# Performance work log

Measured on AMD Instinct MI355X. Metric: run time of the kernel, lower is better.

Reference implementation:

```python
import jax, jax.numpy as jnp
import numpy as np

B, LC, LQ, D = 64, 512, 64, 256

def setup_inputs() -> dict:
    key = jax.random.key(0)
    k1, k2, k3, k4 = jax.random.split(key, 4)
    contex = jax.random.normal(k1, (B, LC, D), dtype=jnp.float32)
    question = jax.random.normal(k2, (B, LQ, D), dtype=jnp.float32)
    W_weight = jax.random.normal(k3, (1, 3 * D), dtype=jnp.float32) * (1.0 / np.sqrt(3 * D))
    W_bias = jax.random.normal(k4, (1,), dtype=jnp.float32) * 0.01
    return {"contex": contex, "question": question, "W_weight": W_weight, "W_bias": W_bias}

def reference(contex, question, W_weight, W_bias):
    d = contex.shape[-1]
    w = W_weight[0]  # [3D]; cat order in original is [q, c, q*c]
    wq, wc, wi = w[:d], w[d:2 * d], w[2 * d:]
    # S[b,i,j] = c_i.wc + q_j.wq + (c_i*q_j).wi + bias  (trilinear decomposition)
    s_c = contex @ wc                                   # [B, Lc]
    s_q = question @ wq                                 # [B, Lq]
    s_i = jnp.einsum('bid,bjd->bij', contex * wi, question)  # [B, Lc, Lq]
    S = s_i + s_c[:, :, None] + s_q[:, None, :] + W_bias[0]
    S1 = jax.nn.softmax(S, axis=2)                      # over question
    S2 = jax.nn.softmax(S, axis=1)                      # over context
    A = jnp.einsum('bij,bjd->bid', S1, question)        # [B, Lc, D]
    S3 = jnp.einsum('bij,bkj->bik', S1, S2)             # [B, Lc, Lc]
    Bm = jnp.einsum('bik,bkd->bid', S3, contex)         # [B, Lc, D]
    out = jnp.concatenate([contex, A, contex * A, contex * Bm], axis=2)  # [B, Lc, 4D]
    return out  # dropout is identity at inference
```

## Files before the change

kernel.cpp:

```cpp
#include <hip/hip_runtime.h>

#define BB 64
#define LCC 512
#define LQQ 64
#define DDD 256

typedef short bf16x8 __attribute__((ext_vector_type(8)));
typedef float f32x4 __attribute__((ext_vector_type(4)));

static __device__ __forceinline__ unsigned short f2bf(float f) {
  union { float f; unsigned u; } v; v.f = f;
  unsigned u = v.u;
  return (unsigned short)((u + 0x7fffu + ((u >> 16) & 1u)) >> 16);
}
static __device__ __forceinline__ float bf2f(unsigned u16) {
  union { unsigned u; float f; } v; v.u = (u16 & 0xffffu) << 16;
  return v.f;
}

__global__ __launch_bounds__(256) void k1_scores(
    const float* __restrict__ cx, const float* __restrict__ qu,
    const float* __restrict__ W, const float* __restrict__ Wb,
    unsigned short* __restrict__ E, unsigned short* __restrict__ Et,
    float* __restrict__ rinv)
{
  __shared__ float w_lds[768];
  __shared__ unsigned short Bs[64 * 264];
  __shared__ float E_lds[64 * 65];
  __shared__ float red[256];
  __shared__ float sc_lds[64];
  __shared__ float sq_lds[64];

  const int tid = threadIdx.x;
  const int b  = blockIdx.x >> 3;
  const int i0 = (blockIdx.x & 7) * 64;
  const int w = tid >> 6, lane = tid & 63, quad = lane >> 4, ln = lane & 15;

  for (int idx = tid; idx < 768; idx += 256) w_lds[idx] = W[idx];
  __syncthreads();

  {
    const int bj = tid >> 2, bc = tid & 3;
    const float4* src = (const float4*)(qu + ((size_t)(b * LQQ + bj)) * DDD + bc * 64);
    const float* wq = w_lds + bc * 64;
    unsigned short* dst = Bs + bj * 264 + bc * 64;
    float sqp = 0.f;
#pragma unroll
    for (int u = 0; u < 16; ++u) {
      float4 v = src[u];
      sqp += v.x * wq[u*4+0] + v.y * wq[u*4+1] + v.z * wq[u*4+2] + v.w * wq[u*4+3];
      ushort4 o = { f2bf(v.x), f2bf(v.y), f2bf(v.z), f2bf(v.w) };
      *(ushort4*)(dst + u * 4) = o;
    }
    red[tid] = sqp;
  }
  __syncthreads();
  if (tid < 64) sq_lds[tid] = red[4*tid] + red[4*tid+1] + red[4*tid+2] + red[4*tid+3];

  f32x4 acc[4];
#pragma unroll
  for (int c = 0; c < 4; ++c) acc[c] = (f32x4){0.f, 0.f, 0.f, 0.f};

  float scp = 0.f;
  const float* cxrow = cx + ((size_t)(b * LCC + i0 + w * 16 + ln)) * DDD;
#pragma unroll
  for (int kk = 0; kk < 4; ++kk)
#pragma unroll
    for (int ks = 0; ks < 2; ++ks) {
      const int k0 = kk * 64 + ks * 32 + quad * 8;
      float4 c0 = *(const float4*)(cxrow + k0);
      float4 c1 = *(const float4*)(cxrow + k0 + 4);
      const float* wcp = w_lds + 256 + k0;
      const float* wip = w_lds + 512 + k0;
      scp += c0.x*wcp[0] + c0.y*wcp[1] + c0.z*wcp[2] + c0.w*wcp[3]
           + c1.x*wcp[4] + c1.y*wcp[5] + c1.z*wcp[6] + c1.w*wcp[7];
      bf16x8 af;
      af[0] = (short)f2bf(c0.x * wip[0]);
      af[1] = (short)f2bf(c0.y * wip[1]);
      af[2] = (short)f2bf(c0.z * wip[2]);
      af[3] = (short)f2bf(c0.w * wip[3]);
      af[4] = (short)f2bf(c1.x * wip[4]);
      af[5] = (short)f2bf(c1.y * wip[5]);
      af[6] = (short)f2bf(c1.z * wip[6]);
      af[7] = (short)f2bf(c1.w * wip[7]);
#pragma unroll
      for (int tn = 0; tn < 4; ++tn) {
        bf16x8 bf = *(const bf16x8*)(Bs + (tn * 16 + ln) * 264 + k0);
        acc[tn] = __builtin_amdgcn_mfma_f32_16x16x32_bf16(af, bf, acc[tn], 0, 0, 0);
      }
    }

  __syncthreads();
  red[(w * 16 + ln) * 4 + quad] = scp;
  __syncthreads();
  if (tid < 64)
    sc_lds[tid] = red[4*tid] + red[4*tid+1] + red[4*tid+2] + red[4*tid+3] + Wb[0];
  __syncthreads();

#pragma unroll
  for (int tn = 0; tn < 4; ++tn)
#pragma unroll
    for (int r = 0; r < 4; ++r) {
      int il = w * 16 + quad * 4 + r;
      int j  = tn * 16 + ln;
      E_lds[il * 65 + j] = __expf(acc[tn][r] + sc_lds[il] + sq_lds[j]);
    }
  __syncthreads();
  {
    const int i = tid >> 2, c = tid & 3;
    float s = 0.f;
#pragma unroll
    for (int j = 0; j < 16; ++j) s += E_lds[i * 65 + c * 16 + j];
    red[tid] = s;
  }
  __syncthreads();
  if (tid < 64)
    rinv[b * LCC + i0 + tid] = 1.0f / (red[4*tid] + red[4*tid+1] + red[4*tid+2] + red[4*tid+3]);

  {
    const int i = tid >> 2, c = tid & 3;
    unsigned short* dst = E + ((size_t)(b * LCC + i0 + i)) * 64 + c * 16;
    const float* srcr = E_lds + i * 65 + c * 16;
#pragma unroll
    for (int u = 0; u < 4; ++u) {
      ushort4 o = { f2bf(srcr[u*4+0]), f2bf(srcr[u*4+1]), f2bf(srcr[u*4+2]), f2bf(srcr[u*4+3]) };
      *(ushort4*)(dst + u * 4) = o;
    }
  }
  {
    const int j = tid >> 2, c = tid & 3;
    unsigned short* dst = Et + ((size_t)(b * LQQ + j)) * LCC + i0 + c * 16;
#pragma unroll
    for (int u = 0; u < 4; ++u) {
      ushort4 o;
      o.x = f2bf(E_lds[(c*16 + u*4 + 0) * 65 + j]);
      o.y = f2bf(E_lds[(c*16 + u*4 + 1) * 65 + j]);
      o.z = f2bf(E_lds[(c*16 + u*4 + 2) * 65 + j]);
      o.w = f2bf(E_lds[(c*16 + u*4 + 3) * 65 + j]);
      *(ushort4*)(dst + u * 4) = o;
    }
  }
}

__global__ __launch_bounds__(256) void k2_tmat(
    const float* __restrict__ cx, const float* __restrict__ qu,
    const unsigned short* __restrict__ Et,
    unsigned short* __restrict__ Qt, unsigned short* __restrict__ Tt)
{
  __shared__ unsigned short Bs2[32 * 72];
  __shared__ float Tl[64 * 37];
  __shared__ float red2[256];
  __shared__ float csinv[64];

  const int tid = threadIdx.x;
  const int b  = blockIdx.x >> 3;
  const int d0 = (blockIdx.x & 7) * 32;
  const int w = tid >> 6, lane = tid & 63, quad = lane >> 4, ln = lane & 15;

  {
    const int j = tid >> 2, c = tid & 3;
    const float* srow = qu + ((size_t)(b * LQQ + j)) * DDD + d0 + c * 8;
    float4 v0 = *(const float4*)srow;
    float4 v1 = *(const float4*)(srow + 4);
    float* t = Tl + j * 37 + c * 8;
    t[0]=v0.x; t[1]=v0.y; t[2]=v0.z; t[3]=v0.w;
    t[4]=v1.x; t[5]=v1.y; t[6]=v1.z; t[7]=v1.w;
  }
  __syncthreads();
  {
    const int d = tid >> 3, cj = tid & 7;
    unsigned short* dst = Qt + ((size_t)(b * DDD + d0 + d)) * 64 + cj * 8;
    ushort4 o0 = { f2bf(Tl[(cj*8+0)*37+d]), f2bf(Tl[(cj*8+1)*37+d]),
                   f2bf(Tl[(cj*8+2)*37+d]), f2bf(Tl[(cj*8+3)*37+d]) };
    ushort4 o1 = { f2bf(Tl[(cj*8+4)*37+d]), f2bf(Tl[(cj*8+5)*37+d]),
                   f2bf(Tl[(cj*8+6)*37+d]), f2bf(Tl[(cj*8+7)*37+d]) };
    *(ushort4*)dst = o0;
    *(ushort4*)(dst + 4) = o1;
  }

  f32x4 acc[2];
  acc[0] = (f32x4){0.f, 0.f, 0.f, 0.f};
  acc[1] = (f32x4){0.f, 0.f, 0.f, 0.f};
  float csp = 0.f;
  const unsigned short* etrow = Et + ((size_t)(b * LQQ + w * 16 + ln)) * LCC;
  const int si = tid & 63, sc2 = tid >> 6;

  for (int kk = 0; kk < 8; ++kk) {
    __syncthreads();
    {
      const float* srow = cx + ((size_t)(b * LCC + kk * 64 + si)) * DDD + d0 + sc2 * 8;
      float4 v0 = *(const float4*)srow;
      float4 v1 = *(const float4*)(srow + 4);
      Bs2[(sc2*8+0)*72 + si] = f2bf(v0.x);
      Bs2[(sc2*8+1)*72 + si] = f2bf(v0.y);
      Bs2[(sc2*8+2)*72 + si] = f2bf(v0.z);
      Bs2[(sc2*8+3)*72 + si] = f2bf(v0.w);
      Bs2[(sc2*8+4)*72 + si] = f2bf(v1.x);
      Bs2[(sc2*8+5)*72 + si] = f2bf(v1.y);
      Bs2[(sc2*8+6)*72 + si] = f2bf(v1.z);
      Bs2[(sc2*8+7)*72 + si] = f2bf(v1.w);
    }
    bf16x8 af0 = *(const bf16x8*)(etrow + kk * 64 + quad * 8);
    bf16x8 af1 = *(const bf16x8*)(etrow + kk * 64 + 32 + quad * 8);
#pragma unroll
    for (int e = 0; e < 8; ++e)
      csp += bf2f((unsigned short)af0[e]) + bf2f((unsigned short)af1[e]);
    __syncthreads();
#pragma unroll
    for (int tn = 0; tn < 2; ++tn) {
      bf16x8 bf0 = *(const bf16x8*)(Bs2 + (tn * 16 + ln) * 72 + quad * 8);
      bf16x8 bf1 = *(const bf16x8*)(Bs2 + (tn * 16 + ln) * 72 + 32 + quad * 8);
      acc[tn] = __builtin_amdgcn_mfma_f32_16x16x32_bf16(af0, bf0, acc[tn], 0, 0, 0);
      acc[tn] = __builtin_amdgcn_mfma_f32_16x16x32_bf16(af1, bf1, acc[tn], 0, 0, 0);
    }
  }

  __syncthreads();
  red2[(w * 16 + ln) * 4 + quad] = csp;
  __syncthreads();
  if (tid < 64)
    csinv[tid] = 1.0f / (red2[4*tid] + red2[4*tid+1] + red2[4*tid+2] + red2[4*tid+3]);
  __syncthreads();
#pragma unroll
  for (int tn = 0; tn < 2; ++tn)
#pragma unroll
    for (int r = 0; r < 4; ++r) {
      int j = w * 16 + quad * 4 + r;
      Tl[j * 37 + tn * 16 + ln] = acc[tn][r] * csinv[j];
    }
  __syncthreads();
  {
    const int d = tid >> 3, cj = tid & 7;
    unsigned short* dst = Tt + ((size_t)(b * DDD + d0 + d)) * 64 + cj * 8;
    ushort4 o0 = { f2bf(Tl[(cj*8+0)*37+d]), f2bf(Tl[(cj*8+1)*37+d]),
                   f2bf(Tl[(cj*8+2)*37+d]), f2bf(Tl[(cj*8+3)*37+d]) };
    ushort4 o1 = { f2bf(Tl[(cj*8+4)*37+d]), f2bf(Tl[(cj*8+5)*37+d]),
                   f2bf(Tl[(cj*8+6)*37+d]), f2bf(Tl[(cj*8+7)*37+d]) };
    *(ushort4*)dst = o0;
    *(ushort4*)(dst + 4) = o1;
  }
}

__global__ __launch_bounds__(256) void k3_out(
    const float* __restrict__ cx,
    const unsigned short* __restrict__ E,
    const unsigned short* __restrict__ Qt,
    const unsigned short* __restrict__ Tt,
    const float* __restrict__ rinv,
    float* __restrict__ out)
{
  __shared__ float Tr[16 * 260];
  __shared__ float ri_lds[64];

  const int tid = threadIdx.x;
  const int bid = blockIdx.x;
  const int b    = bid >> 4;
  const int it   = (bid >> 1) & 7;
  const int half = bid & 1;
  const int i0 = it * 64;
  const int w = tid >> 6, lane = tid & 63, quad = lane >> 4, ln = lane & 15;

  if (tid < 64) ri_lds[tid] = rinv[b * LCC + i0 + tid];

  const unsigned short* Bsrc = (half ? Tt : Qt) + (size_t)b * DDD * 64;
  const unsigned short* ebase = E + ((size_t)(b * LCC + i0)) * 64;

  f32x4 acc[4][4];
#pragma unroll
  for (int a = 0; a < 4; ++a)
#pragma unroll
    for (int c = 0; c < 4; ++c) acc[a][c] = (f32x4){0.f, 0.f, 0.f, 0.f};

#pragma unroll
  for (int ks = 0; ks < 2; ++ks) {
    bf16x8 af[4];
#pragma unroll
    for (int tm = 0; tm < 4; ++tm)
      af[tm] = *(const bf16x8*)(ebase + (tm * 16 + ln) * 64 + ks * 32 + quad * 8);
#pragma unroll
    for (int tn = 0; tn < 4; ++tn) {
      bf16x8 bf = *(const bf16x8*)(Bsrc + ((size_t)(w * 64 + tn * 16 + ln)) * 64 + ks * 32 + quad * 8);
#pragma unroll
      for (int tm = 0; tm < 4; ++tm)
        acc[tm][tn] = __builtin_amdgcn_mfma_f32_16x16x32_bf16(af[tm], bf, acc[tm][tn], 0, 0, 0);
    }
  }

  const float* cxb = cx + (size_t)b * LCC * DDD;
  float* ob = out + (size_t)b * LCC * 1024;
  const int row = tid >> 4;
  const int fq  = tid & 15;

  __syncthreads();
#pragma unroll
  for (int tm = 0; tm < 4; ++tm) {
#pragma unroll
    for (int tn = 0; tn < 4; ++tn)
#pragma unroll
      for (int r = 0; r < 4; ++r) {
        int rloc = quad * 4 + r;
        Tr[rloc * 260 + w * 64 + tn * 16 + ln] = acc[tm][tn][r] * ri_lds[tm * 16 + rloc];
      }
    __syncthreads();
    const int i = i0 + tm * 16 + row;
#pragma unroll
    for (int u = 0; u < 4; ++u) {
      int c0 = (fq + u * 16) * 4;
      float4 v = *(const float4*)(Tr + row * 260 + c0);
      float4 c = *(const float4*)(cxb + (size_t)i * DDD + c0);
      float4 cv = { c.x * v.x, c.y * v.y, c.z * v.z, c.w * v.w };
      if (half == 0) {
        *(float4*)(ob + (size_t)i * 1024 + 256 + c0) = v;
        *(float4*)(ob + (size_t)i * 1024 + 512 + c0) = cv;
      } else {
        *(float4*)(ob + (size_t)i * 1024 + c0)       = c;
        *(float4*)(ob + (size_t)i * 1024 + 768 + c0) = cv;
      }
    }
    __syncthreads();
  }
}

extern "C" void kernel_launch(void* const* d_in, const int* in_sizes, int n_in,
                              void* d_out, int out_size, void* d_ws, size_t ws_size,
                              hipStream_t stream) {
  const float* cx = (const float*)d_in[0];
  const float* qu = (const float*)d_in[1];
  const float* W  = (const float*)d_in[2];
  const float* Wb = (const float*)d_in[3];
  float* out = (float*)d_out;

  char* wsb = (char*)d_ws;
  unsigned short* E   = (unsigned short*)(wsb);
  unsigned short* Et  = (unsigned short*)(wsb + (4ull << 20));
  unsigned short* Qt  = (unsigned short*)(wsb + (8ull << 20));
  unsigned short* Tt  = (unsigned short*)(wsb + (10ull << 20));
  float*          ri  = (float*)(wsb + (12ull << 20));

  k1_scores<<<dim3(512), dim3(256), 0, stream>>>(cx, qu, W, Wb, E, Et, ri);
  k2_tmat  <<<dim3(512), dim3(256), 0, stream>>>(cx, qu, Et, Qt, Tt);
  k3_out   <<<dim3(1024), dim3(256), 0, stream>>>(cx, E, Qt, Tt, ri, out);
}
```

Baseline: 198.7 us.

## Merge k3 halves, fold column sums into k1, write contex copy early

k3 now computes both the A and Bm products in one block, reusing the P tile, and halves the grid. P is stored already row-normalized, so the rinv buffer is no longer needed. Column partial sums of E are computed in k1 and read by k2, which removes k2's per-iteration bf16 summation and its reduction. The contex passthrough slice of the output is written from k1, and all output stores use nontemporal hints. The risks are higher register pressure in k3, with two 4x4 accumulator sets under launch_bounds(256,2), and fewer blocks in flight.

```diff
diff --git a/kernel.cpp b/kernel.cpp
--- a/kernel.cpp
+++ b/kernel.cpp
@@ -13,16 +13,17 @@
   unsigned u = v.u;
   return (unsigned short)((u + 0x7fffu + ((u >> 16) & 1u)) >> 16);
 }
-static __device__ __forceinline__ float bf2f(unsigned u16) {
-  union { unsigned u; float f; } v; v.u = (u16 & 0xffffu) << 16;
-  return v.f;
+
+static __device__ __forceinline__ void nt_store4(float* p, float a, float b, float c, float d) {
+  f32x4 v = { a, b, c, d };
+  __builtin_nontemporal_store(v, (f32x4*)p);
 }
 
 __global__ __launch_bounds__(256) void k1_scores(
     const float* __restrict__ cx, const float* __restrict__ qu,
     const float* __restrict__ W, const float* __restrict__ Wb,
-    unsigned short* __restrict__ E, unsigned short* __restrict__ Et,
-    float* __restrict__ rinv)
+    unsigned short* __restrict__ P, unsigned short* __restrict__ Et,
+    float* __restrict__ csp, float* __restrict__ out)
 {
   __shared__ float w_lds[768];
   __shared__ unsigned short Bs[64 * 264];
@@ -30,10 +31,12 @@
   __shared__ float red[256];
   __shared__ float sc_lds[64];
   __shared__ float sq_lds[64];
+  __shared__ float ri_s[64];
 
   const int tid = threadIdx.x;
-  const int b  = blockIdx.x >> 3;
-  const int i0 = (blockIdx.x & 7) * 64;
+  const int b    = blockIdx.x >> 3;
+  const int tile = blockIdx.x & 7;
+  const int i0 = tile * 64;
   const int w = tid >> 6, lane = tid & 63, quad = lane >> 4, ln = lane & 15;
 
   for (int idx = tid; idx < 768; idx += 256) w_lds[idx] = W[idx];
@@ -63,6 +66,7 @@
 
   float scp = 0.f;
   const float* cxrow = cx + ((size_t)(b * LCC + i0 + w * 16 + ln)) * DDD;
+  float* outrow = out + ((size_t)(b * LCC + i0 + w * 16 + ln)) * 1024;
 #pragma unroll
   for (int kk = 0; kk < 4; ++kk)
 #pragma unroll
@@ -70,6 +74,8 @@
       const int k0 = kk * 64 + ks * 32 + quad * 8;
       float4 c0 = *(const float4*)(cxrow + k0);
       float4 c1 = *(const float4*)(cxrow + k0 + 4);
+      nt_store4(outrow + k0,     c0.x, c0.y, c0.z, c0.w);
+      nt_store4(outrow + k0 + 4, c1.x, c1.y, c1.z, c1.w);
       const float* wcp = w_lds + 256 + k0;
       const float* wip = w_lds + 512 + k0;
       scp += c0.x*wcp[0] + c0.y*wcp[1] + c0.z*wcp[2] + c0.w*wcp[3]
@@ -115,15 +121,29 @@
   }
   __syncthreads();
   if (tid < 64)
-    rinv[b * LCC + i0 + tid] = 1.0f / (red[4*tid] + red[4*tid+1] + red[4*tid+2] + red[4*tid+3]);
+    ri_s[tid] = 1.0f / (red[4*tid] + red[4*tid+1] + red[4*tid+2] + red[4*tid+3]);
+  __syncthreads();
+  {
+    const int j = tid >> 2, c = tid & 3;
+    float s = 0.f;
+#pragma unroll
+    for (int r = 0; r < 16; ++r) s += E_lds[(c * 16 + r) * 65 + j];
+    red[tid] = s;
+  }
+  __syncthreads();
+  if (tid < 64)
+    csp[((size_t)(b * 8 + tile)) * 64 + tid] =
+        red[4*tid] + red[4*tid+1] + red[4*tid+2] + red[4*tid+3];
 
   {
     const int i = tid >> 2, c = tid & 3;
-    unsigned short* dst = E + ((size_t)(b * LCC + i0 + i)) * 64 + c * 16;
+    const float ri = ri_s[i];
+    unsigned short* dst = P + ((size_t)(b * LCC + i0 + i)) * 64 + c * 16;
     const float* srcr = E_lds + i * 65 + c * 16;
 #pragma unroll
     for (int u = 0; u < 4; ++u) {
-      ushort4 o = { f2bf(srcr[u*4+0]), f2bf(srcr[u*4+1]), f2bf(srcr[u*4+2]), f2bf(srcr[u*4+3]) };
+      ushort4 o = { f2bf(srcr[u*4+0]*ri), f2bf(srcr[u*4+1]*ri),
+                    f2bf(srcr[u*4+2]*ri), f2bf(srcr[u*4+3]*ri) };
       *(ushort4*)(dst + u * 4) = o;
     }
   }
@@ -144,12 +164,11 @@
 
 __global__ __launch_bounds__(256) void k2_tmat(
     const float* __restrict__ cx, const float* __restrict__ qu,
-    const unsigned short* __restrict__ Et,
+    const unsigned short* __restrict__ Et, const float* __restrict__ csp,
     unsigned short* __restrict__ Qt, unsigned short* __restrict__ Tt)
 {
   __shared__ unsigned short Bs2[32 * 72];
   __shared__ float Tl[64 * 37];
-  __shared__ float red2[256];
   __shared__ float csinv[64];
 
   const int tid = threadIdx.x;
@@ -178,33 +197,36 @@
     *(ushort4*)(dst + 4) = o1;
   }
 
+  if (tid < 64) {
+    float s = 0.f;
+#pragma unroll
+    for (int t = 0; t < 8; ++t) s += csp[((size_t)(b * 8 + t)) * 64 + tid];
+    csinv[tid] = 1.0f / s;
+  }
+
   f32x4 acc[2];
   acc[0] = (f32x4){0.f, 0.f, 0.f, 0.f};
   acc[1] = (f32x4){0.f, 0.f, 0.f, 0.f};
-  float csp = 0.f;
   const unsigned short* etrow = Et + ((size_t)(b * LQQ + w * 16 + ln)) * LCC;
-  const int si = tid & 63, sc2 = tid >> 6;
+  const int r2 = tid >> 2, c2 = tid & 3;
 
   for (int kk = 0; kk < 8; ++kk) {
     __syncthreads();
     {
-      const float* srow = cx + ((size_t)(b * LCC + kk * 64 + si)) * DDD + d0 + sc2 * 8;
+      const float* srow = cx + ((size_t)(b * LCC + kk * 64 + r2)) * DDD + d0 + c2 * 8;
       float4 v0 = *(const float4*)srow;
       float4 v1 = *(const float4*)(srow + 4);
-      Bs2[(sc2*8+0)*72 + si] = f2bf(v0.x);
-      Bs2[(sc2*8+1)*72 + si] = f2bf(v0.y);
-      Bs2[(sc2*8+2)*72 + si] = f2bf(v0.z);
-      Bs2[(sc2*8+3)*72 + si] = f2bf(v0.w);
-      Bs2[(sc2*8+4)*72 + si] = f2bf(v1.x);
-      Bs2[(sc2*8+5)*72 + si] = f2bf(v1.y);
-      Bs2[(sc2*8+6)*72 + si] = f2bf(v1.z);
-      Bs2[(sc2*8+7)*72 + si] = f2bf(v1.w);
+      Bs2[(c2*8+0)*72 + r2] = f2bf(v0.x);
+      Bs2[(c2*8+1)*72 + r2] = f2bf(v0.y);
+      Bs2[(c2*8+2)*72 + r2] = f2bf(v0.z);
+      Bs2[(c2*8+3)*72 + r2] = f2bf(v0.w);
+      Bs2[(c2*8+4)*72 + r2] = f2bf(v1.x);
+      Bs2[(c2*8+5)*72 + r2] = f2bf(v1.y);
+      Bs2[(c2*8+6)*72 + r2] = f2bf(v1.z);
+      Bs2[(c2*8+7)*72 + r2] = f2bf(v1.w);
     }
     bf16x8 af0 = *(const bf16x8*)(etrow + kk * 64 + quad * 8);
     bf16x8 af1 = *(const bf16x8*)(etrow + kk * 64 + 32 + quad * 8);
-#pragma unroll
-    for (int e = 0; e < 8; ++e)
-      csp += bf2f((unsigned short)af0[e]) + bf2f((unsigned short)af1[e]);
     __syncthreads();
 #pragma unroll
     for (int tn = 0; tn < 2; ++tn) {
@@ -215,12 +237,6 @@
     }
   }
 
-  __syncthreads();
-  red2[(w * 16 + ln) * 4 + quad] = csp;
-  __syncthreads();
-  if (tid < 64)
-    csinv[tid] = 1.0f / (red2[4*tid] + red2[4*tid+1] + red2[4*tid+2] + red2[4*tid+3]);
-  __syncthreads();
 #pragma unroll
   for (int tn = 0; tn < 2; ++tn)
 #pragma unroll
@@ -241,48 +257,50 @@
   }
 }
 
-__global__ __launch_bounds__(256) void k3_out(
+__global__ __launch_bounds__(256, 2) void k3_out(
     const float* __restrict__ cx,
-    const unsigned short* __restrict__ E,
+    const unsigned short* __restrict__ P,
     const unsigned short* __restrict__ Qt,
     const unsigned short* __restrict__ Tt,
-    const float* __restrict__ rinv,
     float* __restrict__ out)
 {
-  __shared__ float Tr[16 * 260];
-  __shared__ float ri_lds[64];
+  __shared__ float TrA[16 * 260];
+  __shared__ float TrB[16 * 260];
 
   const int tid = threadIdx.x;
-  const int bid = blockIdx.x;
-  const int b    = bid >> 4;
-  const int it   = (bid >> 1) & 7;
-  const int half = bid & 1;
-  const int i0 = it * 64;
+  const int b  = blockIdx.x >> 3;
+  const int i0 = (blockIdx.x & 7) * 64;
   const int w = tid >> 6, lane = tid & 63, quad = lane >> 4, ln = lane & 15;
 
-  if (tid < 64) ri_lds[tid] = rinv[b * LCC + i0 + tid];
-
-  const unsigned short* Bsrc = (half ? Tt : Qt) + (size_t)b * DDD * 64;
-  const unsigned short* ebase = E + ((size_t)(b * LCC + i0)) * 64;
-
-  f32x4 acc[4][4];
+  const unsigned short* pbase = P + ((size_t)(b * LCC + i0)) * 64;
+  const unsigned short* qbase = Qt + (size_t)b * DDD * 64;
+  const unsigned short* tbase = Tt + (size_t)b * DDD * 64;
+
+  f32x4 accA[4][4], accB[4][4];
 #pragma unroll
   for (int a = 0; a < 4; ++a)
 #pragma unroll
-    for (int c = 0; c < 4; ++c) acc[a][c] = (f32x4){0.f, 0.f, 0.f, 0.f};
+    for (int c = 0; c < 4; ++c) {
+      accA[a][c] = (f32x4){0.f, 0.f, 0.f, 0.f};
+      accB[a][c] = (f32x4){0.f, 0.f, 0.f, 0.f};
+    }
 
 #pragma unroll
   for (int ks = 0; ks < 2; ++ks) {
     bf16x8 af[4];
 #pragma unroll
     for (int tm = 0; tm < 4; ++tm)
-      af[tm] = *(const bf16x8*)(ebase + (tm * 16 + ln) * 64 + ks * 32 + quad * 8);
+      af[tm] = *(const bf16x8*)(pbase + (tm * 16 + ln) * 64 + ks * 32 + quad * 8);
 #pragma unroll
     for (int tn = 0; tn < 4; ++tn) {
-      bf16x8 bf = *(const bf16x8*)(Bsrc + ((size_t)(w * 64 + tn * 16 + ln)) * 64 + ks * 32 + quad * 8);
-#pragma unroll
-      for (int tm = 0; tm < 4; ++tm)
-        acc[tm][tn] = __builtin_amdgcn_mfma_f32_16x16x32_bf16(af[tm], bf, acc[tm][tn], 0, 0, 0);
+      const size_t boff = ((size_t)(w * 64 + tn * 16 + ln)) * 64 + ks * 32 + quad * 8;
+      bf16x8 bq = *(const bf16x8*)(qbase + boff);
+      bf16x8 bt = *(const bf16x8*)(tbase + boff);
+#pragma unroll
+      for (int tm = 0; tm < 4; ++tm) {
+        accA[tm][tn] = __builtin_amdgcn_mfma_f32_16x16x32_bf16(af[tm], bq, accA[tm][tn], 0, 0, 0);
+        accB[tm][tn] = __builtin_amdgcn_mfma_f32_16x16x32_bf16(af[tm], bt, accB[tm][tn], 0, 0, 0);
+      }
     }
   }
 
@@ -291,7 +309,6 @@
   const int row = tid >> 4;
   const int fq  = tid & 15;
 
-  __syncthreads();
 #pragma unroll
   for (int tm = 0; tm < 4; ++tm) {
 #pragma unroll
@@ -299,23 +316,20 @@
 #pragma unroll
       for (int r = 0; r < 4; ++r) {
         int rloc = quad * 4 + r;
-        Tr[rloc * 260 + w * 64 + tn * 16 + ln] = acc[tm][tn][r] * ri_lds[tm * 16 + rloc];
+        TrA[rloc * 260 + w * 64 + tn * 16 + ln] = accA[tm][tn][r];
+        TrB[rloc * 260 + w * 64 + tn * 16 + ln] = accB[tm][tn][r];
       }
     __syncthreads();
     const int i = i0 + tm * 16 + row;
 #pragma unroll
     for (int u = 0; u < 4; ++u) {
       int c0 = (fq + u * 16) * 4;
-      float4 v = *(const float4*)(Tr + row * 260 + c0);
-      float4 c = *(const float4*)(cxb + (size_t)i * DDD + c0);
-      float4 cv = { c.x * v.x, c.y * v.y, c.z * v.z, c.w * v.w };
-      if (half == 0) {
-        *(float4*)(ob + (size_t)i * 1024 + 256 + c0) = v;
-        *(float4*)(ob + (size_t)i * 1024 + 512 + c0) = cv;
-      } else {
-        *(float4*)(ob + (size_t)i * 1024 + c0)       = c;
-        *(float4*)(ob + (size_t)i * 1024 + 768 + c0) = cv;
-      }
+      float4 a  = *(const float4*)(TrA + row * 260 + c0);
+      float4 bm = *(const float4*)(TrB + row * 260 + c0);
+      float4 c  = *(const float4*)(cxb + (size_t)i * DDD + c0);
+      nt_store4(ob + (size_t)i * 1024 + 256 + c0, a.x, a.y, a.z, a.w);
+      nt_store4(ob + (size_t)i * 1024 + 512 + c0, c.x*a.x, c.y*a.y, c.z*a.z, c.w*a.w);
+      nt_store4(ob + (size_t)i * 1024 + 768 + c0, c.x*bm.x, c.y*bm.y, c.z*bm.z, c.w*bm.w);
     }
     __syncthreads();
   }
@@ -331,13 +345,13 @@
   float* out = (float*)d_out;
 
   char* wsb = (char*)d_ws;
-  unsigned short* E   = (unsigned short*)(wsb);
+  unsigned short* P   = (unsigned short*)(wsb);
   unsigned short* Et  = (unsigned short*)(wsb + (4ull << 20));
   unsigned short* Qt  = (unsigned short*)(wsb + (8ull << 20));
   unsigned short* Tt  = (unsigned short*)(wsb + (10ull << 20));
-  float*          ri  = (float*)(wsb + (12ull << 20));
-
-  k1_scores<<<dim3(512), dim3(256), 0, stream>>>(cx, qu, W, Wb, E, Et, ri);
-  k2_tmat  <<<dim3(512), dim3(256), 0, stream>>>(cx, qu, Et, Qt, Tt);
-  k3_out   <<<dim3(1024), dim3(256), 0, stream>>>(cx, E, Qt, Tt, ri, out);
-}
+  float*          csp = (float*)(wsb + (12ull << 20));
+
+  k1_scores<<<dim3(512), dim3(256), 0, stream>>>(cx, qu, W, Wb, P, Et, csp, out);
+  k2_tmat  <<<dim3(512), dim3(256), 0, stream>>>(cx, qu, Et, csp, Qt, Tt);
+  k3_out   <<<dim3(512), dim3(256), 0, stream>>>(cx, P, Qt, Tt, out);
+}
```

New measurement: 208.7 us. +5.0%, slower.
